# Kernel optimization log

Hardware: AMD Instinct MI355X
Metric: run time of the kernel (lower is better)

The kernel has to match this reference:

```python
import jax, jax.numpy as jnp
import numpy as np

B, N, NFEAT, NHID, NOUT, NMLP, NCLASS = 32, 1024, 128, 64, 64, 128, 2
ALPHA = 0.2  # leaky relu slope
NEG = -9e15


def setup_inputs() -> dict:
    key = jax.random.key(0)
    ks = jax.random.split(key, 12)
    x = jax.random.normal(ks[0], (B, N, NFEAT), dtype=jnp.float32)
    x_mask = (jax.random.uniform(ks[1], (B, N)) < 0.9).astype(jnp.float32)
    adj = (jax.random.uniform(ks[2], (B, N, N)) < 0.05).astype(jnp.float32)
    adj = jnp.maximum(adj, jnp.eye(N, dtype=jnp.float32)[None])  # self loops
    s = 0.02
    W0 = jax.random.normal(ks[3], (NFEAT, NHID), dtype=jnp.float32) * s
    a0 = jax.random.normal(ks[4], (2 * NHID, 1), dtype=jnp.float32) * s
    Wout = jax.random.normal(ks[5], (NHID, NOUT), dtype=jnp.float32) * s
    aout = jax.random.normal(ks[6], (2 * NOUT, 1), dtype=jnp.float32) * s
    W1 = jax.random.normal(ks[7], (NOUT, NMLP), dtype=jnp.float32) * s
    b1 = jnp.zeros((NMLP,), dtype=jnp.float32)
    W2 = jax.random.normal(ks[8], (NMLP, NCLASS), dtype=jnp.float32) * s
    b2 = jnp.zeros((NCLASS,), dtype=jnp.float32)
    return {"x": x, "x_mask": x_mask, "adj": adj, "W0": W0, "a0": a0,
            "Wout": Wout, "aout": aout, "W1": W1, "b1": b1, "W2": W2, "b2": b2}


def _gat_layer(h, adj, W, a):
    # h: [B,N,F_in], W: [F_in,F_out], a: [2*F_out,1]
    Wh = jnp.einsum('bnf,fh->bnh', h, W)                 # [B,N,F_out]
    d = W.shape[1]
    f1 = Wh @ a[:d]                                      # [B,N,1]
    f2 = Wh @ a[d:]                                      # [B,N,1]
    e = jax.nn.leaky_relu(f1 + jnp.swapaxes(f2, 1, 2), ALPHA)  # [B,N,N]
    e = jnp.where(adj > 0, e, NEG)
    attn = jax.nn.softmax(e, axis=-1)
    return jnp.einsum('bnm,bmh->bnh', attn, Wh)


def reference(x, x_mask, adj, W0, a0, Wout, aout, W1, b1, W2, b2):
    # Only head 0 reaches out_att in the original (zip truncation); dropout is
    # identity in eval mode.
    h = jax.nn.elu(_gat_layer(x, adj, W0, a0))           # concat=True -> elu
    h = jax.nn.elu(_gat_layer(h, adj, Wout, aout))       # F.elu applied outside
    m = x_mask[..., None]
    g = jnp.sum(h * m, axis=1) / jnp.maximum(jnp.sum(x_mask, axis=1, keepdims=True), 1.0)  # masked mean readout [B,NOUT]
    return jax.nn.relu(g @ W1 + b1) @ W2 + b2            # [B,NCLASS]
```

## Files before the change

kernel.cpp:

```cpp
#include <hip/hip_runtime.h>
#include <math.h>

#define BB 32
#define NN 1024
#define NFEAT 128
#define ALPHA 0.2f
#define MAXD 128

#define WH1_TILE_BLOCKS (BB * NN / 64)
#define ATTN_BLOCKS (BB * NN / 8)

__device__ __forceinline__ void gld_f4(float4& d, const float* a) {
  asm volatile("global_load_dwordx4 %0, %1, off" : "=v"(d) : "v"(a));
}

template<int FIN>
__device__ __forceinline__ void wh_tile_body(
    const int blk, const int tid,
    const float* __restrict__ hin, const float* __restrict__ W,
    const float* __restrict__ a, float* __restrict__ Wh,
    float* __restrict__ f1, float* __restrict__ f2) {
  const int tx = tid & 15;
  const int ty = tid >> 4;
  const int row0 = blk * 64 + ty * 4;

  float4 acc[4];
#pragma unroll
  for (int i = 0; i < 4; ++i) acc[i] = make_float4(0.f, 0.f, 0.f, 0.f);

#pragma unroll 4
  for (int k = 0; k < FIN; k += 4) {
    float4 wv[4];
#pragma unroll
    for (int i = 0; i < 4; ++i)
      wv[i] = *reinterpret_cast<const float4*>(&W[(size_t)(k + i) * 64 + tx * 4]);
#pragma unroll
    for (int i = 0; i < 4; ++i) {
      const float4 xv = *reinterpret_cast<const float4*>(
          &hin[(size_t)(row0 + i) * FIN + k]);
      acc[i].x = fmaf(xv.x, wv[0].x, acc[i].x);
      acc[i].y = fmaf(xv.x, wv[0].y, acc[i].y);
      acc[i].z = fmaf(xv.x, wv[0].z, acc[i].z);
      acc[i].w = fmaf(xv.x, wv[0].w, acc[i].w);
      acc[i].x = fmaf(xv.y, wv[1].x, acc[i].x);
      acc[i].y = fmaf(xv.y, wv[1].y, acc[i].y);
      acc[i].z = fmaf(xv.y, wv[1].z, acc[i].z);
      acc[i].w = fmaf(xv.y, wv[1].w, acc[i].w);
      acc[i].x = fmaf(xv.z, wv[2].x, acc[i].x);
      acc[i].y = fmaf(xv.z, wv[2].y, acc[i].y);
      acc[i].z = fmaf(xv.z, wv[2].z, acc[i].z);
      acc[i].w = fmaf(xv.z, wv[2].w, acc[i].w);
      acc[i].x = fmaf(xv.w, wv[3].x, acc[i].x);
      acc[i].y = fmaf(xv.w, wv[3].y, acc[i].y);
      acc[i].z = fmaf(xv.w, wv[3].z, acc[i].z);
      acc[i].w = fmaf(xv.w, wv[3].w, acc[i].w);
    }
  }

  const float4 av1 = *reinterpret_cast<const float4*>(&a[tx * 4]);
  const float4 av2 = *reinterpret_cast<const float4*>(&a[64 + tx * 4]);
#pragma unroll
  for (int i = 0; i < 4; ++i) {
    const int row = row0 + i;
    *reinterpret_cast<float4*>(&Wh[(size_t)row * 64 + tx * 4]) = acc[i];
    float c1 = acc[i].x * av1.x + acc[i].y * av1.y + acc[i].z * av1.z + acc[i].w * av1.w;
    float c2 = acc[i].x * av2.x + acc[i].y * av2.y + acc[i].z * av2.z + acc[i].w * av2.w;
#pragma unroll
    for (int off = 8; off > 0; off >>= 1) {
      c1 += __shfl_xor(c1, off, 64);
      c2 += __shfl_xor(c2, off, 64);
    }
    if (tx == 0) { f1[row] = c1; f2[row] = c2; }
  }
}

__global__ __launch_bounds__(256) void wh1_kernel(
    const float* __restrict__ x, const float* __restrict__ W0,
    const float* __restrict__ a0, float* __restrict__ Wh,
    float* __restrict__ f1, float* __restrict__ f2) {
  wh_tile_body<NFEAT>(blockIdx.x, threadIdx.x, x, W0, a0, Wh, f1, f2);
}

__device__ __forceinline__ void gather4(
    const float* ps0, const unsigned short* ms0,
    const float* ps1, const unsigned short* ms1,
    const int bound, const float* __restrict__ Whb,
    const int slot, const int fq, float4& outA, float4& outB) {
  float4 accA = make_float4(0.f, 0.f, 0.f, 0.f);
  float4 accB = make_float4(0.f, 0.f, 0.f, 0.f);
  const float* WhF = Whb + fq * 4;
  for (int k = 0; k < bound; k += 4) {
    const int ia = ms0[k + slot];
    const int ib = ms1[k + slot];
    const float pa = ps0[k + slot];
    const float pb = ps1[k + slot];
    const float4 wa = *reinterpret_cast<const float4*>(&WhF[(size_t)ia * 64]);
    const float4 wb = *reinterpret_cast<const float4*>(&WhF[(size_t)ib * 64]);
    accA.x = fmaf(pa, wa.x, accA.x);
    accA.y = fmaf(pa, wa.y, accA.y);
    accA.z = fmaf(pa, wa.z, accA.z);
    accA.w = fmaf(pa, wa.w, accA.w);
    accB.x = fmaf(pb, wb.x, accB.x);
    accB.y = fmaf(pb, wb.y, accB.y);
    accB.z = fmaf(pb, wb.z, accB.z);
    accB.w = fmaf(pb, wb.w, accB.w);
  }
#pragma unroll
  for (int off = 16; off <= 32; off <<= 1) {
    accA.x += __shfl_xor(accA.x, off, 64);
    accA.y += __shfl_xor(accA.y, off, 64);
    accA.z += __shfl_xor(accA.z, off, 64);
    accA.w += __shfl_xor(accA.w, off, 64);
    accB.x += __shfl_xor(accB.x, off, 64);
    accB.y += __shfl_xor(accB.y, off, 64);
    accB.z += __shfl_xor(accB.z, off, 64);
    accB.w += __shfl_xor(accB.w, off, 64);
  }
  outA = accA;
  outB = accB;
}

__device__ __forceinline__ float4 elu4(const float4 v) {
  return make_float4(v.x > 0.f ? v.x : expm1f(v.x),
                     v.y > 0.f ? v.y : expm1f(v.y),
                     v.z > 0.f ? v.z : expm1f(v.z),
                     v.w > 0.f ? v.w : expm1f(v.w));
}

__global__ __launch_bounds__(256) void scan_attn1_kernel(
    const float* __restrict__ adj,
    const float* __restrict__ f1, const float* __restrict__ f2,
    const float* __restrict__ Wh,
    const float* __restrict__ Wnext, const float* __restrict__ anext,
    unsigned short* __restrict__ nbr, int* __restrict__ cnt,
    float* __restrict__ WhOut, float* __restrict__ f1o,
    float* __restrict__ f2o) {
  __shared__ __align__(16) float ps[4][2][MAXD];
  __shared__ __align__(16) unsigned short msh[4][2][MAXD];
  __shared__ __align__(16) float h1s[4][2][64];
  const int wv = threadIdx.x >> 6, lane = threadIdx.x & 63;
  const int slot = lane >> 4, fq = lane & 15;
  const int j = blockIdx.x;
  const int batch = (j & 7) + 8 * (j >> 10);
  const int cp = (j >> 3) & 127;
  const int row0 = (batch * 256 + 2 * cp) * 4 + wv;

  const float f1v0 = f1[row0];
  const float f1v1 = f1[row0 + 4];
  const float* f2b = f2 + (size_t)batch * NN;

  const float* ar0 = adj + (size_t)row0 * NN + lane * 4;
  const float* ar1 = adj + (size_t)(row0 + 4) * NN + lane * 4;
  float4 av00, av01, av02, av03, av10, av11, av12, av13;
  gld_f4(av00, ar0);        gld_f4(av01, ar0 + 256);
  gld_f4(av02, ar0 + 512);  gld_f4(av03, ar0 + 768);
  gld_f4(av10, ar1);        gld_f4(av11, ar1 + 256);
  gld_f4(av12, ar1 + 512);  gld_f4(av13, ar1 + 768);

  msh[wv][0][lane] = 0;  msh[wv][0][64 + lane] = 0;
  msh[wv][1][lane] = 0;  msh[wv][1][64 + lane] = 0;

  asm volatile("s_waitcnt vmcnt(0)" ::: "memory");
  __builtin_amdgcn_sched_barrier(0);

  const unsigned long long lmask = (1ull << lane) - 1ull;
  auto compact = [&](const float4& c0, const float4& c1, const float4& c2,
                     const float4& c3, unsigned short* mrow) -> int {
    int count = 0;
#pragma unroll
    for (int c = 0; c < 4; ++c) {
      const float4& cv = (c == 0) ? c0 : (c == 1) ? c1 : (c == 2) ? c2 : c3;
      const int m = (cv.x > 0.f ? 1 : 0) | (cv.y > 0.f ? 2 : 0) |
                    (cv.z > 0.f ? 4 : 0) | (cv.w > 0.f ? 8 : 0);
      const unsigned long long b0 = __ballot(m & 1);
      const unsigned long long b1 = __ballot(m & 2);
      const unsigned long long b2 = __ballot(m & 4);
      const unsigned long long b3 = __ballot(m & 8);
      int base = count + __popcll(b0 & lmask) + __popcll(b1 & lmask) +
                 __popcll(b2 & lmask) + __popcll(b3 & lmask);
      const int e0 = c * 256 + lane * 4;
      if (m & 1) { if (base < MAXD) mrow[base] = (unsigned short)(e0);     ++base; }
      if (m & 2) { if (base < MAXD) mrow[base] = (unsigned short)(e0 + 1); ++base; }
      if (m & 4) { if (base < MAXD) mrow[base] = (unsigned short)(e0 + 2); ++base; }
      if (m & 8) { if (base < MAXD) mrow[base] = (unsigned short)(e0 + 3); ++base; }
      count += __popcll(b0) + __popcll(b1) + __popcll(b2) + __popcll(b3);
    }
    return count < MAXD ? count : MAXD;
  };
  const int count0 = compact(av00, av01, av02, av03, msh[wv][0]);
  const int count1 = compact(av10, av11, av12, av13, msh[wv][1]);
  if (lane == 0) { cnt[row0] = count0; cnt[row0 + 4] = count1; }
  {
    const unsigned lo0 = msh[wv][0][2 * lane];
    const unsigned hi0 = msh[wv][0][2 * lane + 1];
    reinterpret_cast<unsigned*>(nbr + (size_t)row0 * MAXD)[lane] = lo0 | (hi0 << 16);
    const unsigned lo1 = msh[wv][1][2 * lane];
    const unsigned hi1 = msh[wv][1][2 * lane + 1];
    reinterpret_cast<unsigned*>(nbr + (size_t)(row0 + 4) * MAXD)[lane] = lo1 | (hi1 << 16);
  }

#pragma unroll
  for (int rr = 0; rr < 2; ++rr) {
    const int cntr = rr == 0 ? count0 : count1;
    const float f1n = rr == 0 ? f1v0 : f1v1;
    const int m0 = msh[wv][rr][lane];
    const int m1 = msh[wv][rr][64 + lane];
    const bool on0 = lane < cntr, on1 = 64 + lane < cntr;
    const float v0 = f1n + f2b[m0];
    const float v1 = f1n + f2b[m1];
    float e0v = on0 ? (v0 > 0.f ? v0 : ALPHA * v0) : -3e38f;
    float e1v = on1 ? (v1 > 0.f ? v1 : ALPHA * v1) : -3e38f;
    float lmax = fmaxf(e0v, e1v);
#pragma unroll
    for (int off = 32; off > 0; off >>= 1) lmax = fmaxf(lmax, __shfl_xor(lmax, off, 64));
    const float p0 = on0 ? __expf(e0v - lmax) : 0.f;
    const float p1 = on1 ? __expf(e1v - lmax) : 0.f;
    float ls = p0 + p1;
#pragma unroll
    for (int off = 32; off > 0; off >>= 1) ls += __shfl_xor(ls, off, 64);
    const float inv = 1.f / ls;
    ps[wv][rr][lane] = p0 * inv;
    ps[wv][rr][64 + lane] = p1 * inv;
  }

  const int cmax = count0 > count1 ? count0 : count1;
  const int bound = (cmax + 3) & ~3;
  const float* Whb = Wh + (size_t)batch * (NN * 64);
  float4 accA, accB;
  gather4(ps[wv][0], msh[wv][0], ps[wv][1], msh[wv][1], bound, Whb,
          slot, fq, accA, accB);
  if (slot == 0) {
    *reinterpret_cast<float4*>(&h1s[wv][0][fq * 4]) = elu4(accA);
    *reinterpret_cast<float4*>(&h1s[wv][1][fq * 4]) = elu4(accB);
  }

  float s0 = 0.f, s1 = 0.f;
#pragma unroll 8
  for (int f = 0; f < 64; ++f) {
    const float w = Wnext[f * 64 + lane];
    s0 = fmaf(h1s[wv][0][f], w, s0);
    s1 = fmaf(h1s[wv][1][f], w, s1);
  }
  WhOut[(size_t)row0 * 64 + lane] = s0;
  WhOut[(size_t)(row0 + 4) * 64 + lane] = s1;
  const float a1v = anext[lane], a2v = anext[64 + lane];
  float c10 = s0 * a1v, c20 = s0 * a2v;
  float c11 = s1 * a1v, c21 = s1 * a2v;
#pragma unroll
  for (int off = 32; off > 0; off >>= 1) {
    c10 += __shfl_xor(c10, off, 64);
    c20 += __shfl_xor(c20, off, 64);
    c11 += __shfl_xor(c11, off, 64);
    c21 += __shfl_xor(c21, off, 64);
  }
  if (lane == 0) {
    f1o[row0] = c10;  f2o[row0] = c20;
    f1o[row0 + 4] = c11;  f2o[row0 + 4] = c21;
  }
}

__global__ __launch_bounds__(256) void attn2_kernel(
    const unsigned short* __restrict__ nbr, const int* __restrict__ cnt,
    const float* __restrict__ f1, const float* __restrict__ f2,
    const float* __restrict__ Wh, const float* __restrict__ mask,
    float* __restrict__ part2) {
  __shared__ __align__(16) float ps[4][2][MAXD];
  __shared__ __align__(16) unsigned short msh[4][2][MAXD];
  __shared__ __align__(16) float agg[4][2][64];
  const int wv = threadIdx.x >> 6, lane = threadIdx.x & 63;
  const int slot = lane >> 4, fq = lane & 15;
  const int j = blockIdx.x;
  const int batch = (j & 7) + 8 * (j >> 10);
  const int cp = (j >> 3) & 127;
  const int row0 = (batch * 256 + 2 * cp) * 4 + wv;

  const float* f2b = f2 + (size_t)batch * NN;
  const float f1v[2] = { f1[row0], f1[row0 + 4] };
  int count_r[2];
#pragma unroll
  for (int rr = 0; rr < 2; ++rr) {
    int cntr = cnt[row0 + rr * 4];
    if (cntr > MAXD) cntr = MAXD;
    count_r[rr] = cntr;
    const unsigned short* nrow = nbr + (size_t)(row0 + rr * 4) * MAXD;
    const int m0 = nrow[lane];
    const int m1 = nrow[64 + lane];
    const bool on0 = lane < cntr, on1 = 64 + lane < cntr;
    const float v0 = f1v[rr] + f2b[m0];
    const float v1 = f1v[rr] + f2b[m1];
    float e0v = on0 ? (v0 > 0.f ? v0 : ALPHA * v0) : -3e38f;
    float e1v = on1 ? (v1 > 0.f ? v1 : ALPHA * v1) : -3e38f;
    float lmax = fmaxf(e0v, e1v);
#pragma unroll
    for (int off = 32; off > 0; off >>= 1) lmax = fmaxf(lmax, __shfl_xor(lmax, off, 64));
    const float p0 = on0 ? __expf(e0v - lmax) : 0.f;
    const float p1 = on1 ? __expf(e1v - lmax) : 0.f;
    float ls = p0 + p1;
#pragma unroll
    for (int off = 32; off > 0; off >>= 1) ls += __shfl_xor(ls, off, 64);
    const float inv = 1.f / ls;
    ps[wv][rr][lane] = p0 * inv;
    ps[wv][rr][64 + lane] = p1 * inv;
    msh[wv][rr][lane] = (unsigned short)(on0 ? m0 : 0);
    msh[wv][rr][64 + lane] = (unsigned short)(on1 ? m1 : 0);
  }

  const int cmax = count_r[0] > count_r[1] ? count_r[0] : count_r[1];
  const int bound = (cmax + 3) & ~3;
  const float* Whb = Wh + (size_t)batch * (NN * 64);
  float4 accA, accB;
  gather4(ps[wv][0], msh[wv][0], ps[wv][1], msh[wv][1], bound, Whb,
          slot, fq, accA, accB);
  const float mv0 = mask[row0];
  const float mv1 = mask[row0 + 4];
  if (slot == 0) {
    const float4 h0 = elu4(accA);
    const float4 h1 = elu4(accB);
    *reinterpret_cast<float4*>(&agg[wv][0][fq * 4]) =
        make_float4(mv0 * h0.x, mv0 * h0.y, mv0 * h0.z, mv0 * h0.w);
    *reinterpret_cast<float4*>(&agg[wv][1][fq * 4]) =
        make_float4(mv1 * h1.x, mv1 * h1.y, mv1 * h1.z, mv1 * h1.w);
  }
  __syncthreads();
  if (wv < 2)
    part2[((size_t)batch * 256 + 2 * cp + wv) * 64 + lane] =
        (agg[0][wv][lane] + agg[1][wv][lane]) +
        (agg[2][wv][lane] + agg[3][wv][lane]);
}

__global__ __launch_bounds__(256) void mlp2_kernel(
    const float* __restrict__ part2, const float* __restrict__ mask,
    const float* __restrict__ W1, const float* __restrict__ b1,
    const float* __restrict__ W2, const float* __restrict__ b2,
    float* __restrict__ outp) {
  const int b = blockIdx.x;
  const int tid = threadIdx.x;
  const int wv = tid >> 6, lane = tid & 63;
  __shared__ float aggG[4][64];
  __shared__ float msW[4];
  __shared__ float g[64];
  __shared__ float hid[128];

  const float4 mv4 = *reinterpret_cast<const float4*>(&mask[(size_t)b * NN + tid * 4]);
  float ms = (mv4.x + mv4.y) + (mv4.z + mv4.w);
#pragma unroll
  for (int off = 32; off > 0; off >>= 1) ms += __shfl_xor(ms, off, 64);
  if (lane == 0) msW[wv] = ms;

  float gs = 0.f;
  const float* pb = part2 + ((size_t)b * 256 + wv * 64) * 64 + lane;
#pragma unroll 8
  for (int i = 0; i < 64; ++i) gs += pb[(size_t)i * 64];
  aggG[wv][lane] = gs;
  __syncthreads();
  const float denom = fmaxf((msW[0] + msW[1]) + (msW[2] + msW[3]), 1.0f);
  if (tid < 64)
    g[tid] = ((aggG[0][tid] + aggG[1][tid]) + (aggG[2][tid] + aggG[3][tid])) / denom;
  __syncthreads();
  if (tid < 128) {
    float s = b1[tid];
#pragma unroll 8
    for (int k = 0; k < 64; ++k) s += g[k] * W1[k * 128 + tid];
    hid[tid] = fmaxf(s, 0.f);
  }
  __syncthreads();
  if (tid < 2) {
    float o = b2[tid];
    for (int jj = 0; jj < 128; ++jj) o += hid[jj] * W2[jj * 2 + tid];
    outp[b * 2 + tid] = o;
  }
}

extern "C" void kernel_launch(void* const* d_in, const int* in_sizes, int n_in,
                              void* d_out, int out_size, void* d_ws, size_t ws_size,
                              hipStream_t stream) {
  const float* x      = (const float*)d_in[0];
  const float* x_mask = (const float*)d_in[1];
  const float* adj    = (const float*)d_in[2];
  const float* W0     = (const float*)d_in[3];
  const float* a0     = (const float*)d_in[4];
  const float* Wout   = (const float*)d_in[5];
  const float* aout   = (const float*)d_in[6];
  const float* W1     = (const float*)d_in[7];
  const float* b1     = (const float*)d_in[8];
  const float* W2     = (const float*)d_in[9];
  const float* b2     = (const float*)d_in[10];
  float* out = (float*)d_out;

  const int rows = BB * NN;

  float* ws = (float*)d_ws;
  float* Wh  = ws;
  float* Wh2 = Wh + (size_t)rows * 64;
  float* f1  = Wh2 + (size_t)rows * 64;
  float* f2  = f1 + rows;
  float* f1b = f2 + rows;
  float* f2b = f1b + rows;
  int*   cnt = (int*)(f2b + rows);
  unsigned short* nbr = (unsigned short*)(cnt + rows);
  float* part2 = (float*)(nbr + (size_t)rows * MAXD);

  wh1_kernel<<<WH1_TILE_BLOCKS, 256, 0, stream>>>(x, W0, a0, Wh, f1, f2);
  scan_attn1_kernel<<<ATTN_BLOCKS, 256, 0, stream>>>(
      adj, f1, f2, Wh, Wout, aout, nbr, cnt, Wh2, f1b, f2b);
  attn2_kernel<<<ATTN_BLOCKS, 256, 0, stream>>>(
      nbr, cnt, f1b, f2b, Wh2, x_mask, part2);
  mlp2_kernel<<<BB, 256, 0, stream>>>(part2, x_mask, W1, b1, W2, b2, out);
}
```

Before: 101.8 us.

## Replace neighbor-list handoff with adjacency bitmask and per-kernel bit compaction

Adds a separate kernel that turns the float adjacency matrix into a 16-bit-per-lane bitmask. Both attention kernels then rebuild the neighbor lists from that bitmask with a popcount prefix scan and ffs loop. This replaces the scan fused into the first attention kernel and the stored neighbor-index/count arrays. The adjacency read (the largest memory traffic) now sits in a simple streaming kernel, at the cost of an extra launch, compaction done twice, and loss of the overlap between the adjacency scan and attention.

```diff
diff --git a/kernel.cpp b/kernel.cpp
--- a/kernel.cpp
+++ b/kernel.cpp
@@ -8,11 +8,8 @@
 #define MAXD 128
 
 #define WH1_TILE_BLOCKS (BB * NN / 64)
+#define BM_BLOCKS (BB * NN / 4)
 #define ATTN_BLOCKS (BB * NN / 8)
-
-__device__ __forceinline__ void gld_f4(float4& d, const float* a) {
-  asm volatile("global_load_dwordx4 %0, %1, off" : "=v"(d) : "v"(a));
-}
 
 template<int FIN>
 __device__ __forceinline__ void wh_tile_body(
@@ -79,6 +76,49 @@
     const float* __restrict__ a0, float* __restrict__ Wh,
     float* __restrict__ f1, float* __restrict__ f2) {
   wh_tile_body<NFEAT>(blockIdx.x, threadIdx.x, x, W0, a0, Wh, f1, f2);
+}
+
+__global__ __launch_bounds__(256) void bitmask_kernel(
+    const float* __restrict__ adj, unsigned short* __restrict__ bm) {
+  const int wv = threadIdx.x >> 6, lane = threadIdx.x & 63;
+  const int row = blockIdx.x * 4 + wv;
+  const float* ar = adj + (size_t)row * NN + lane * 16;
+  const float4 a0 = *reinterpret_cast<const float4*>(ar);
+  const float4 a1 = *reinterpret_cast<const float4*>(ar + 4);
+  const float4 a2 = *reinterpret_cast<const float4*>(ar + 8);
+  const float4 a3 = *reinterpret_cast<const float4*>(ar + 12);
+  unsigned m = 0;
+  m |= (a0.x > 0.f ? 1u : 0u);        m |= (a0.y > 0.f ? 2u : 0u);
+  m |= (a0.z > 0.f ? 4u : 0u);        m |= (a0.w > 0.f ? 8u : 0u);
+  m |= (a1.x > 0.f ? 16u : 0u);       m |= (a1.y > 0.f ? 32u : 0u);
+  m |= (a1.z > 0.f ? 64u : 0u);       m |= (a1.w > 0.f ? 128u : 0u);
+  m |= (a2.x > 0.f ? 256u : 0u);      m |= (a2.y > 0.f ? 512u : 0u);
+  m |= (a2.z > 0.f ? 1024u : 0u);     m |= (a2.w > 0.f ? 2048u : 0u);
+  m |= (a3.x > 0.f ? 4096u : 0u);     m |= (a3.y > 0.f ? 8192u : 0u);
+  m |= (a3.z > 0.f ? 16384u : 0u);    m |= (a3.w > 0.f ? 32768u : 0u);
+  bm[(size_t)row * 64 + lane] = (unsigned short)m;
+}
+
+__device__ __forceinline__ int bit_compact(
+    const unsigned short* __restrict__ bmrow, unsigned short* msh,
+    const int lane) {
+  unsigned w = bmrow[lane];
+  const int myc = __popc(w);
+  int pre = myc;
+#pragma unroll
+  for (int off = 1; off < 64; off <<= 1) {
+    const int v = __shfl_up(pre, off, 64);
+    if (lane >= off) pre += v;
+  }
+  const int total = __shfl(pre, 63, 64);
+  int base = pre - myc;
+  while (w) {
+    const int b = __ffs(w) - 1;
+    if (base < MAXD) msh[base] = (unsigned short)(lane * 16 + b);
+    w &= w - 1;
+    ++base;
+  }
+  return total < MAXD ? total : MAXD;
 }
 
 __device__ __forceinline__ void gather4(
@@ -127,12 +167,11 @@
                      v.w > 0.f ? v.w : expm1f(v.w));
 }
 
-__global__ __launch_bounds__(256) void scan_attn1_kernel(
-    const float* __restrict__ adj,
+__global__ __launch_bounds__(256) void attn1_kernel(
+    const unsigned short* __restrict__ bm,
     const float* __restrict__ f1, const float* __restrict__ f2,
     const float* __restrict__ Wh,
     const float* __restrict__ Wnext, const float* __restrict__ anext,
-    unsigned short* __restrict__ nbr, int* __restrict__ cnt,
     float* __restrict__ WhOut, float* __restrict__ f1o,
     float* __restrict__ f2o) {
   __shared__ __align__(16) float ps[4][2][MAXD];
@@ -145,60 +184,14 @@
   const int cp = (j >> 3) & 127;
   const int row0 = (batch * 256 + 2 * cp) * 4 + wv;
 
+  msh[wv][0][lane] = 0;  msh[wv][0][64 + lane] = 0;
+  msh[wv][1][lane] = 0;  msh[wv][1][64 + lane] = 0;
+  const int count0 = bit_compact(bm + (size_t)row0 * 64, msh[wv][0], lane);
+  const int count1 = bit_compact(bm + (size_t)(row0 + 4) * 64, msh[wv][1], lane);
+
   const float f1v0 = f1[row0];
   const float f1v1 = f1[row0 + 4];
   const float* f2b = f2 + (size_t)batch * NN;
-
-  const float* ar0 = adj + (size_t)row0 * NN + lane * 4;
-  const float* ar1 = adj + (size_t)(row0 + 4) * NN + lane * 4;
-  float4 av00, av01, av02, av03, av10, av11, av12, av13;
-  gld_f4(av00, ar0);        gld_f4(av01, ar0 + 256);
-  gld_f4(av02, ar0 + 512);  gld_f4(av03, ar0 + 768);
-  gld_f4(av10, ar1);        gld_f4(av11, ar1 + 256);
-  gld_f4(av12, ar1 + 512);  gld_f4(av13, ar1 + 768);
-
-  msh[wv][0][lane] = 0;  msh[wv][0][64 + lane] = 0;
-  msh[wv][1][lane] = 0;  msh[wv][1][64 + lane] = 0;
-
-  asm volatile("s_waitcnt vmcnt(0)" ::: "memory");
-  __builtin_amdgcn_sched_barrier(0);
-
-  const unsigned long long lmask = (1ull << lane) - 1ull;
-  auto compact = [&](const float4& c0, const float4& c1, const float4& c2,
-                     const float4& c3, unsigned short* mrow) -> int {
-    int count = 0;
-#pragma unroll
-    for (int c = 0; c < 4; ++c) {
-      const float4& cv = (c == 0) ? c0 : (c == 1) ? c1 : (c == 2) ? c2 : c3;
-      const int m = (cv.x > 0.f ? 1 : 0) | (cv.y > 0.f ? 2 : 0) |
-                    (cv.z > 0.f ? 4 : 0) | (cv.w > 0.f ? 8 : 0);
-      const unsigned long long b0 = __ballot(m & 1);
-      const unsigned long long b1 = __ballot(m & 2);
-      const unsigned long long b2 = __ballot(m & 4);
-      const unsigned long long b3 = __ballot(m & 8);
-      int base = count + __popcll(b0 & lmask) + __popcll(b1 & lmask) +
-                 __popcll(b2 & lmask) + __popcll(b3 & lmask);
-      const int e0 = c * 256 + lane * 4;
-      if (m & 1) { if (base < MAXD) mrow[base] = (unsigned short)(e0);     ++base; }
-      if (m & 2) { if (base < MAXD) mrow[base] = (unsigned short)(e0 + 1); ++base; }
-      if (m & 4) { if (base < MAXD) mrow[base] = (unsigned short)(e0 + 2); ++base; }
-      if (m & 8) { if (base < MAXD) mrow[base] = (unsigned short)(e0 + 3); ++base; }
-      count += __popcll(b0) + __popcll(b1) + __popcll(b2) + __popcll(b3);
-    }
-    return count < MAXD ? count : MAXD;
-  };
-  const int count0 = compact(av00, av01, av02, av03, msh[wv][0]);
-  const int count1 = compact(av10, av11, av12, av13, msh[wv][1]);
-  if (lane == 0) { cnt[row0] = count0; cnt[row0 + 4] = count1; }
-  {
-    const unsigned lo0 = msh[wv][0][2 * lane];
-    const unsigned hi0 = msh[wv][0][2 * lane + 1];
-    reinterpret_cast<unsigned*>(nbr + (size_t)row0 * MAXD)[lane] = lo0 | (hi0 << 16);
-    const unsigned lo1 = msh[wv][1][2 * lane];
-    const unsigned hi1 = msh[wv][1][2 * lane + 1];
-    reinterpret_cast<unsigned*>(nbr + (size_t)(row0 + 4) * MAXD)[lane] = lo1 | (hi1 << 16);
-  }
-
 #pragma unroll
   for (int rr = 0; rr < 2; ++rr) {
     const int cntr = rr == 0 ? count0 : count1;
@@ -260,7 +253,7 @@
 }
 
 __global__ __launch_bounds__(256) void attn2_kernel(
-    const unsigned short* __restrict__ nbr, const int* __restrict__ cnt,
+    const unsigned short* __restrict__ bm,
     const float* __restrict__ f1, const float* __restrict__ f2,
     const float* __restrict__ Wh, const float* __restrict__ mask,
     float* __restrict__ part2) {
@@ -274,17 +267,18 @@
   const int cp = (j >> 3) & 127;
   const int row0 = (batch * 256 + 2 * cp) * 4 + wv;
 
+  msh[wv][0][lane] = 0;  msh[wv][0][64 + lane] = 0;
+  msh[wv][1][lane] = 0;  msh[wv][1][64 + lane] = 0;
+  const int count0 = bit_compact(bm + (size_t)row0 * 64, msh[wv][0], lane);
+  const int count1 = bit_compact(bm + (size_t)(row0 + 4) * 64, msh[wv][1], lane);
+
   const float* f2b = f2 + (size_t)batch * NN;
   const float f1v[2] = { f1[row0], f1[row0 + 4] };
-  int count_r[2];
 #pragma unroll
   for (int rr = 0; rr < 2; ++rr) {
-    int cntr = cnt[row0 + rr * 4];
-    if (cntr > MAXD) cntr = MAXD;
-    count_r[rr] = cntr;
-    const unsigned short* nrow = nbr + (size_t)(row0 + rr * 4) * MAXD;
-    const int m0 = nrow[lane];
-    const int m1 = nrow[64 + lane];
+    const int cntr = rr == 0 ? count0 : count1;
+    const int m0 = msh[wv][rr][lane];
+    const int m1 = msh[wv][rr][64 + lane];
     const bool on0 = lane < cntr, on1 = 64 + lane < cntr;
     const float v0 = f1v[rr] + f2b[m0];
     const float v1 = f1v[rr] + f2b[m1];
@@ -301,11 +295,9 @@
     const float inv = 1.f / ls;
     ps[wv][rr][lane] = p0 * inv;
     ps[wv][rr][64 + lane] = p1 * inv;
-    msh[wv][rr][lane] = (unsigned short)(on0 ? m0 : 0);
-    msh[wv][rr][64 + lane] = (unsigned short)(on1 ? m1 : 0);
-  }
-
-  const int cmax = count_r[0] > count_r[1] ? count_r[0] : count_r[1];
+  }
+
+  const int cmax = count0 > count1 ? count0 : count1;
   const int bound = (cmax + 3) & ~3;
   const float* Whb = Wh + (size_t)batch * (NN * 64);
   float4 accA, accB;
@@ -396,14 +388,14 @@
   float* f2  = f1 + rows;
   float* f1b = f2 + rows;
   float* f2b = f1b + rows;
-  int*   cnt = (int*)(f2b + rows);
-  unsigned short* nbr = (unsigned short*)(cnt + rows);
-  float* part2 = (float*)(nbr + (size_t)rows * MAXD);
-
+  unsigned short* bm = (unsigned short*)(f2b + rows);
+  float* part2 = (float*)(bm + (size_t)rows * 64);
+
+  bitmask_kernel<<<BM_BLOCKS, 256, 0, stream>>>(adj, bm);
   wh1_kernel<<<WH1_TILE_BLOCKS, 256, 0, stream>>>(x, W0, a0, Wh, f1, f2);
-  scan_attn1_kernel<<<ATTN_BLOCKS, 256, 0, stream>>>(
-      adj, f1, f2, Wh, Wout, aout, nbr, cnt, Wh2, f1b, f2b);
+  attn1_kernel<<<ATTN_BLOCKS, 256, 0, stream>>>(
+      bm, f1, f2, Wh, Wout, aout, Wh2, f1b, f2b);
   attn2_kernel<<<ATTN_BLOCKS, 256, 0, stream>>>(
-      nbr, cnt, f1b, f2b, Wh2, x_mask, part2);
+      bm, f1b, f2b, Wh2, x_mask, part2);
   mlp2_kernel<<<BB, 256, 0, stream>>>(part2, x_mask, W1, b1, W2, b2, out);
 }
```

New measurement: 113.1 us. 1.11x slower.
